# Optimization experiments

Hardware: AMD Instinct MI355X
Metric: run time of the kernel (lower is better)

The kernel has to match this reference:

```python
import jax, jax.numpy as jnp
import numpy as np

EMBED = 1024

def setup_inputs() -> dict:
    key = jax.random.key(0)
    ks = jax.random.split(key, 7)
    s = 1.0 / np.sqrt(EMBED)
    x = jax.random.normal(ks[0], (8, 2048, EMBED), dtype=jnp.float32)
    Wk = jax.random.uniform(ks[1], (EMBED, EMBED), jnp.float32, -s, s)
    bk = jax.random.uniform(ks[2], (EMBED,), jnp.float32, -s, s)
    Wq = jax.random.uniform(ks[3], (EMBED, EMBED), jnp.float32, -s, s)
    bq = jax.random.uniform(ks[4], (EMBED,), jnp.float32, -s, s)
    Wv = jax.random.uniform(ks[5], (EMBED, EMBED), jnp.float32, -s, s)
    bv = jax.random.uniform(ks[6], (EMBED,), jnp.float32, -s, s)
    return {"x": x, "Wq": Wq, "bq": bq, "Wk": Wk, "bk": bk, "Wv": Wv, "bv": bv}

def reference(x, Wq, bq, Wk, bk, Wv, bv):
    # Linear projections (PyTorch Linear: y = x @ W^T + b; W here stored as [in, out] = W^T)
    Q = x @ Wq + bq          # [b, s, d]
    K = x @ Wk + bk
    V = x @ Wv + bv
    scale = 1.0 / jnp.sqrt(jnp.asarray(x.shape[-1], x.dtype))
    scores = jnp.einsum('bqd,bkd->bqk', Q, K) * scale  # [b, s, s]
    attn = jax.nn.softmax(scores, axis=-1)
    return jnp.einsum('bqk,bkd->bqd', attn, V)
```

## Files before the change

### kernel.cpp

```cpp
#include <hip/hip_runtime.h>

typedef __attribute__((ext_vector_type(4))) float f32x4;
typedef __attribute__((ext_vector_type(8))) short bf16x8;
typedef __attribute__((ext_vector_type(4))) unsigned short u16x4;

static __device__ __forceinline__ unsigned short f2bf(float f) {
    union { float f; unsigned int u; } a; a.f = f;
    unsigned int u = a.u;
    unsigned int r = (u + 0x7FFFu + ((u >> 16) & 1u)) >> 16;
    return (unsigned short)r;
}
static __device__ __forceinline__ float bf2f(unsigned short h) {
    union { unsigned int u; float f; } a; a.u = ((unsigned int)h) << 16;
    return a.f;
}
static __device__ __forceinline__ unsigned lds_off(const void* p) {
    return (unsigned)(unsigned long long)(const __attribute__((address_space(3))) void*)p;
}

__global__ __launch_bounds__(256) void cvt_f32_bf16(const float* __restrict__ in,
                                                    unsigned short* __restrict__ out) {
    long long i = ((long long)blockIdx.x * 256 + threadIdx.x) * 4;
    float4 f = *(const float4*)(in + i);
    u16x4 u;
    u[0] = f2bf(f.x); u[1] = f2bf(f.y); u[2] = f2bf(f.z); u[3] = f2bf(f.w);
    *(u16x4*)(out + i) = u;
}

__global__ __launch_bounds__(256) void transpose_w(const float* __restrict__ W0,
                                                   const float* __restrict__ W1,
                                                   const float* __restrict__ W2,
                                                   unsigned short* __restrict__ Wt) {
    __shared__ float t[32][33];
    int mat = blockIdx.z;
    const float* W = (mat == 0) ? W0 : (mat == 1) ? W1 : W2;
    unsigned short* out = Wt + (long long)mat * 1024 * 1024;
    int n0 = blockIdx.x * 32, k0 = blockIdx.y * 32;
    int tx = threadIdx.x, ty = threadIdx.y;
#pragma unroll
    for (int q = 0; q < 4; ++q)
        t[ty + 8 * q][tx] = W[(long long)(k0 + ty + 8 * q) * 1024 + n0 + tx];
    __syncthreads();
#pragma unroll
    for (int q = 0; q < 4; ++q)
        out[(long long)(n0 + ty + 8 * q) * 1024 + k0 + tx] = f2bf(t[tx][ty + 8 * q]);
}

#define GBM 256
#define GBN 256

template<int OUT_MODE, int BIAS_MODE>
__global__ __launch_bounds__(512, 2) void gemm8p(
    const unsigned short* __restrict__ A, int lda, long long strideA,
    const unsigned short* __restrict__ B, int ldb, long long strideB,
    void* __restrict__ Cv, int ldc, long long strideC,
    const float* __restrict__ bias, int K, float scale)
{
    __shared__ __align__(16) char lds[131072];

    const int gx = gridDim.x, gy = gridDim.y;
    int lin = blockIdx.x + gx * (blockIdx.y + gy * blockIdx.z);
    const int nwg = gx * gy * gridDim.z;
    const int qch = nwg >> 3;
    int swz = (lin & 7) * qch + (lin >> 3);
    const int bx = swz % gx; int t2 = swz / gx;
    const int by = t2 % gy;  const int bz = t2 / gy;

    const unsigned short* Ag = A + (long long)bz * strideA;
    const unsigned short* Bg = B + (long long)bz * strideB;
    const int m0 = by * GBM, n0 = bx * GBN;

    const int tid  = threadIdx.x;
    const int lane = tid & 63, w = tid >> 6;
    const int wm = w >> 2, wn = w & 3;
    const int l15 = lane & 15, l4 = lane >> 4;

    const int sr = lane >> 3;
    const int ss = (lane & 7) ^ sr;
    const unsigned short* Asrc = Ag + (long long)(m0 + w * 8 + sr) * lda + ss * 8;
    const unsigned short* Bsrc = Bg + (long long)(n0 + w * 8 + sr) * ldb + ss * 8;

    f32x4 acc[8][4] = {};

    auto stageA = [&](int p, int kt, int h) {
#pragma unroll
        for (int i = 0; i < 2; ++i)
            __builtin_amdgcn_global_load_lds(
                (const __attribute__((address_space(1))) void*)(Asrc + (long long)(h * 128 + i * 64) * lda + kt),
                (__attribute__((address_space(3))) void*)(lds + p * 32768 + (h * 128 + i * 64 + w * 8) * 128), 16, 0, 0);
    };
    auto stageB = [&](int p, int kt, int h) {
#pragma unroll
        for (int i = 0; i < 2; ++i)
            __builtin_amdgcn_global_load_lds(
                (const __attribute__((address_space(1))) void*)(Bsrc + (long long)(h * 128 + i * 64) * ldb + kt),
                (__attribute__((address_space(3))) void*)(lds + 65536 + p * 32768 + (h * 128 + i * 64 + w * 8) * 128), 16, 0, 0);
    };

    const unsigned ldsb = lds_off(lds);
    const unsigned as0  = (unsigned)(((l4    ) ^ (l15 & 7)) * 16);
    const unsigned as1  = (unsigned)(((l4 + 4) ^ (l15 & 7)) * 16);
    const unsigned aRow = (unsigned)((wm * 128 + l15) * 128);
    const unsigned bRow = (unsigned)((wn * 64 + l15) * 128);

    bf16x8 a0[4], a1[4], b0[4], b1[4];
    auto readA = [&](bf16x8 (&af)[4], int p, int mh, int ks) {
        unsigned base = ldsb + (unsigned)(p * 32768) + aRow + (unsigned)(mh * 8192) + (ks ? as1 : as0);
#pragma unroll
        for (int fi = 0; fi < 4; ++fi) {
            unsigned off = base + (unsigned)(fi * 2048);
            asm volatile("ds_read_b128 %0, %1" : "=v"(af[fi]) : "v"(off));
        }
    };
    auto readB = [&](bf16x8 (&bf)[4], int p, int ks) {
        unsigned base = ldsb + 65536u + (unsigned)(p * 32768) + bRow + (ks ? as1 : as0);
#pragma unroll
        for (int nj = 0; nj < 4; ++nj) {
            unsigned off = base + (unsigned)(nj * 2048);
            asm volatile("ds_read_b128 %0, %1" : "=v"(bf[nj]) : "v"(off));
        }
    };
    auto mfma16 = [&](int mh, bf16x8 (&af)[4], bf16x8 (&bf)[4]) {
#pragma unroll
        for (int fi = 0; fi < 4; ++fi)
#pragma unroll
            for (int nj = 0; nj < 4; ++nj)
                acc[mh * 4 + fi][nj] = __builtin_amdgcn_mfma_f32_16x16x32_bf16(
                    af[fi], bf[nj], acc[mh * 4 + fi][nj], 0, 0, 0);
    };

#define VMCNT2 asm volatile("s_waitcnt vmcnt(2)" ::: "memory")
#define VMCNT0 asm volatile("s_waitcnt vmcnt(0)" ::: "memory")
#define LGKM0  asm volatile("s_waitcnt lgkmcnt(0)" ::: "memory")
#define SCHED0 __builtin_amdgcn_sched_barrier(0)
#define BARR   __builtin_amdgcn_s_barrier()
#define PRIO1  __builtin_amdgcn_s_setprio(1)
#define PRIO0  __builtin_amdgcn_s_setprio(0)

    const int NT = K >> 6;
    stageA(0, 0, 0); stageA(0, 0, 1); stageB(0, 0, 0); stageB(0, 0, 1);
    stageA(1, 64, 0);
    VMCNT2; BARR; SCHED0;

    for (int t = 0; t < NT; ++t) {
        const int p = t & 1, q = p ^ 1;
        const int kt1 = (t + 1) << 6, kt2 = (t + 2) << 6;
        const bool s1 = (t + 1) < NT, s2 = (t + 2) < NT;
        readA(a0, p, 0, 0); readB(b0, p, 0);
        if (s1) stageB(q, kt1, 0);
        BARR; LGKM0; SCHED0; PRIO1; mfma16(0, a0, b0); PRIO0; BARR;
        readA(a1, p, 1, 0);
        if (s1) stageA(q, kt1, 1);
        BARR; LGKM0; SCHED0; PRIO1; mfma16(1, a1, b0); PRIO0; BARR;
        readA(a0, p, 0, 1); readB(b1, p, 1);
        if (s1) stageB(q, kt1, 1);
        BARR; LGKM0; SCHED0; PRIO1; mfma16(0, a0, b1); PRIO0; BARR;
        readA(a1, p, 1, 1);
        if (s2) stageA(p, kt2, 0);
        if (t == NT - 1) { VMCNT0; } else { VMCNT2; }
        BARR; LGKM0; SCHED0; PRIO1; mfma16(1, a1, b1); PRIO0; BARR;
    }

    const float* bias_v = bias;
    asm volatile("" : "+s"(bias_v));
    unsigned short* Cb = (unsigned short*)Cv;
    float* Cf = (float*)Cv;
    long long cbase = (long long)bz * strideC;
#pragma unroll
    for (int mh = 0; mh < 2; ++mh)
#pragma unroll
    for (int fi = 0; fi < 4; ++fi) {
#pragma unroll
        for (int nj = 0; nj < 4; ++nj) {
            int n = n0 + wn * 64 + nj * 16 + l15;
            float bn = (BIAS_MODE == 1) ? bias_v[n] : 0.0f;
#pragma unroll
            for (int r = 0; r < 4; ++r) {
                int m = m0 + wm * 128 + mh * 64 + fi * 16 + l4 * 4 + r;
                float v = acc[mh * 4 + fi][nj][r] * scale + bn;
                if (BIAS_MODE == 2) v += bias_v[m];
                long long idx = cbase + (long long)m * ldc + n;
                if (OUT_MODE == 0) Cb[idx] = f2bf(v);
                else               Cf[idx] = v;
            }
        }
    }
}

__global__ __launch_bounds__(256) void softmax_rows_bf16(unsigned short* __restrict__ S) {
    int row  = blockIdx.x * 4 + (threadIdx.x >> 6);
    int lane = threadIdx.x & 63;
    unsigned short* Srow = S + (long long)row * 2048;
    float v[32];
    float mx = -1e30f;
#pragma unroll
    for (int j = 0; j < 4; ++j) {
        bf16x8 h = *(const bf16x8*)(Srow + j * 512 + lane * 8);
#pragma unroll
        for (int e = 0; e < 8; ++e) {
            float f = bf2f((unsigned short)h[e]);
            v[j * 8 + e] = f;
            mx = fmaxf(mx, f);
        }
    }
#pragma unroll
    for (int o = 32; o; o >>= 1) mx = fmaxf(mx, __shfl_xor(mx, o));
    float sum = 0.0f;
#pragma unroll
    for (int e = 0; e < 32; ++e) {
        v[e] = __expf(v[e] - mx);
        sum += v[e];
    }
#pragma unroll
    for (int o = 32; o; o >>= 1) sum += __shfl_xor(sum, o);
    float inv = 1.0f / sum;
#pragma unroll
    for (int j = 0; j < 4; ++j) {
        bf16x8 h;
#pragma unroll
        for (int e = 0; e < 8; ++e) h[e] = (short)f2bf(v[j * 8 + e] * inv);
        *(bf16x8*)(Srow + j * 512 + lane * 8) = h;
    }
}

extern "C" void kernel_launch(void* const* d_in, const int* in_sizes, int n_in,
                              void* d_out, int out_size, void* d_ws, size_t ws_size,
                              hipStream_t stream) {
    (void)in_sizes; (void)n_in; (void)out_size; (void)ws_size;
    const float* x  = (const float*)d_in[0];
    const float* Wq = (const float*)d_in[1];
    const float* bq = (const float*)d_in[2];
    const float* Wk = (const float*)d_in[3];
    const float* bk = (const float*)d_in[4];
    const float* Wv = (const float*)d_in[5];
    const float* bv = (const float*)d_in[6];

    char* ws = (char*)d_ws;
    unsigned short* Wt  = (unsigned short*)ws;
    unsigned short* Qb  = (unsigned short*)(ws + 6291456);
    unsigned short* Kb  = (unsigned short*)(ws + 39845888);
    unsigned short* Vt  = (unsigned short*)(ws + 73400320);
    unsigned short* xb  = (unsigned short*)(ws + 106954752);
    unsigned short* Sb  = (unsigned short*)(ws + 106954752);

    cvt_f32_bf16<<<dim3(16384), dim3(256), 0, stream>>>(x, xb);
    transpose_w<<<dim3(32, 32, 3), dim3(32, 8), 0, stream>>>(Wq, Wk, Wv, Wt);

    gemm8p<0, 1><<<dim3(4, 64, 1), dim3(512), 0, stream>>>(
        xb, 1024, 0, Wt, 1024, 0, Qb, 1024, 0, bq, 1024, 1.0f);
    gemm8p<0, 1><<<dim3(4, 64, 1), dim3(512), 0, stream>>>(
        xb, 1024, 0, Wt + 1048576, 1024, 0, Kb, 1024, 0, bk, 1024, 1.0f);
    gemm8p<0, 2><<<dim3(64, 4, 1), dim3(512), 0, stream>>>(
        Wt + 2097152, 1024, 0, xb, 1024, 0, Vt, 16384, 0, bv, 1024, 1.0f);

    gemm8p<0, 0><<<dim3(8, 8, 8), dim3(512), 0, stream>>>(
        Qb, 1024, 2097152LL, Kb, 1024, 2097152LL,
        Sb, 2048, 4194304LL, nullptr, 1024, 0.03125f);

    softmax_rows_bf16<<<dim3(4096), dim3(256), 0, stream>>>(Sb);

    gemm8p<1, 0><<<dim3(4, 8, 8), dim3(512), 0, stream>>>(
        Sb, 2048, 4194304LL,
        Vt, 16384, 2048LL,
        d_out, 1024, 2097152LL, nullptr, 2048, 1.0f);
}
```

Before: 285.8 us.

## Restructure GEMM main loop to one barrier per k-tile with overlapped LDS reads

Replaces the four-phase per-k-tile loop, which had paired barriers around each MFMA block and staggered async global-to-LDS staging, with a simpler ping-pong scheme. Each k-tile now waits for all outstanding global loads, takes one barrier, issues the whole next tile's staging, then streams LDS reads into four separate A-fragment register sets with partial lgkmcnt waits so MFMAs start before all reads land. The aim is fewer barriers and better overlap of LDS reads with MFMA. In exchange it uses more registers, and the full vmcnt(0) wait at the top of each tile removes the earlier prefetch lead, which may expose global-load latency.

Result: faster. 275.3 us (-3.7%).

```diff
diff --git a/kernel.cpp b/kernel.cpp
--- a/kernel.cpp
+++ b/kernel.cpp
@@ -50,7 +50,7 @@
 #define GBN 256
 
 template<int OUT_MODE, int BIAS_MODE>
-__global__ __launch_bounds__(512, 2) void gemm8p(
+__global__ __launch_bounds__(512, 2) void gemmpp(
     const unsigned short* __restrict__ A, int lda, long long strideA,
     const unsigned short* __restrict__ B, int ldb, long long strideB,
     void* __restrict__ Cv, int ldc, long long strideC,
@@ -103,7 +103,7 @@
     const unsigned aRow = (unsigned)((wm * 128 + l15) * 128);
     const unsigned bRow = (unsigned)((wn * 64 + l15) * 128);
 
-    bf16x8 a0[4], a1[4], b0[4], b1[4];
+    bf16x8 aA[4], aB[4], aC[4], aD[4], bA[4], bB[4];
     auto readA = [&](bf16x8 (&af)[4], int p, int mh, int ks) {
         unsigned base = ldsb + (unsigned)(p * 32768) + aRow + (unsigned)(mh * 8192) + (ks ? as1 : as0);
 #pragma unroll
@@ -129,8 +129,9 @@
                     af[fi], bf[nj], acc[mh * 4 + fi][nj], 0, 0, 0);
     };
 
-#define VMCNT2 asm volatile("s_waitcnt vmcnt(2)" ::: "memory")
 #define VMCNT0 asm volatile("s_waitcnt vmcnt(0)" ::: "memory")
+#define LGKM8  asm volatile("s_waitcnt lgkmcnt(8)" ::: "memory")
+#define LGKM4  asm volatile("s_waitcnt lgkmcnt(4)" ::: "memory")
 #define LGKM0  asm volatile("s_waitcnt lgkmcnt(0)" ::: "memory")
 #define SCHED0 __builtin_amdgcn_sched_barrier(0)
 #define BARR   __builtin_amdgcn_s_barrier()
@@ -139,26 +140,24 @@
 
     const int NT = K >> 6;
     stageA(0, 0, 0); stageA(0, 0, 1); stageB(0, 0, 0); stageB(0, 0, 1);
-    stageA(1, 64, 0);
-    VMCNT2; BARR; SCHED0;
 
     for (int t = 0; t < NT; ++t) {
         const int p = t & 1, q = p ^ 1;
-        const int kt1 = (t + 1) << 6, kt2 = (t + 2) << 6;
-        const bool s1 = (t + 1) < NT, s2 = (t + 2) < NT;
-        readA(a0, p, 0, 0); readB(b0, p, 0);
-        if (s1) stageB(q, kt1, 0);
-        BARR; LGKM0; SCHED0; PRIO1; mfma16(0, a0, b0); PRIO0; BARR;
-        readA(a1, p, 1, 0);
-        if (s1) stageA(q, kt1, 1);
-        BARR; LGKM0; SCHED0; PRIO1; mfma16(1, a1, b0); PRIO0; BARR;
-        readA(a0, p, 0, 1); readB(b1, p, 1);
-        if (s1) stageB(q, kt1, 1);
-        BARR; LGKM0; SCHED0; PRIO1; mfma16(0, a0, b1); PRIO0; BARR;
-        readA(a1, p, 1, 1);
-        if (s2) stageA(p, kt2, 0);
-        if (t == NT - 1) { VMCNT0; } else { VMCNT2; }
-        BARR; LGKM0; SCHED0; PRIO1; mfma16(1, a1, b1); PRIO0; BARR;
+        VMCNT0; BARR; SCHED0;
+        if (t + 1 < NT) {
+            const int kt1 = (t + 1) << 6;
+            stageA(q, kt1, 0); stageA(q, kt1, 1);
+            stageB(q, kt1, 0); stageB(q, kt1, 1);
+        }
+        SCHED0;
+        readA(aA, p, 0, 0); readB(bA, p, 0);
+        readA(aB, p, 1, 0);
+        LGKM4; SCHED0; PRIO1; mfma16(0, aA, bA); PRIO0;
+        readA(aC, p, 0, 1); readB(bB, p, 1);
+        LGKM8; SCHED0; PRIO1; mfma16(1, aB, bA); PRIO0;
+        readA(aD, p, 1, 1);
+        LGKM4; SCHED0; PRIO1; mfma16(0, aC, bB); PRIO0;
+        LGKM0; SCHED0; PRIO1; mfma16(1, aD, bB); PRIO0;
     }
 
     const float* bias_v = bias;
@@ -246,20 +245,20 @@
     cvt_f32_bf16<<<dim3(16384), dim3(256), 0, stream>>>(x, xb);
     transpose_w<<<dim3(32, 32, 3), dim3(32, 8), 0, stream>>>(Wq, Wk, Wv, Wt);
 
-    gemm8p<0, 1><<<dim3(4, 64, 1), dim3(512), 0, stream>>>(
+    gemmpp<0, 1><<<dim3(4, 64, 1), dim3(512), 0, stream>>>(
         xb, 1024, 0, Wt, 1024, 0, Qb, 1024, 0, bq, 1024, 1.0f);
-    gemm8p<0, 1><<<dim3(4, 64, 1), dim3(512), 0, stream>>>(
+    gemmpp<0, 1><<<dim3(4, 64, 1), dim3(512), 0, stream>>>(
         xb, 1024, 0, Wt + 1048576, 1024, 0, Kb, 1024, 0, bk, 1024, 1.0f);
-    gemm8p<0, 2><<<dim3(64, 4, 1), dim3(512), 0, stream>>>(
+    gemmpp<0, 2><<<dim3(64, 4, 1), dim3(512), 0, stream>>>(
         Wt + 2097152, 1024, 0, xb, 1024, 0, Vt, 16384, 0, bv, 1024, 1.0f);
 
-    gemm8p<0, 0><<<dim3(8, 8, 8), dim3(512), 0, stream>>>(
+    gemmpp<0, 0><<<dim3(8, 8, 8), dim3(512), 0, stream>>>(
         Qb, 1024, 2097152LL, Kb, 1024, 2097152LL,
         Sb, 2048, 4194304LL, nullptr, 1024, 0.03125f);
 
     softmax_rows_bf16<<<dim3(4096), dim3(256), 0, stream>>>(Sb);
 
-    gemm8p<1, 0><<<dim3(4, 8, 8), dim3(512), 0, stream>>>(
+    gemmpp<1, 0><<<dim3(4, 8, 8), dim3(512), 0, stream>>>(
         Sb, 2048, 4194304LL,
         Vt, 16384, 2048LL,
         d_out, 1024, 2097152LL, nullptr, 2048, 1.0f);
```
